# Optimization experiments

Hardware: AMD Instinct MI355X
Metric: run time of the kernel (lower is better)

Reference implementation:

```python
import jax, jax.numpy as jnp
import numpy as np

B, S, DIN, DIM = 4, 4096, 256, 256
GAMMA = 0.9865


def setup_inputs() -> dict:
    key = jax.random.key(0)
    ks = jax.random.split(key, 9)
    inp = {
        'xq': jax.random.normal(ks[0], (B, S, DIN), dtype=jnp.float32),
        'xk': jax.random.normal(ks[1], (B, S, DIN), dtype=jnp.float32),
        'xv': jax.random.normal(ks[2], (B, S, DIN), dtype=jnp.float32),
        'Wq': jax.random.normal(ks[3], (DIN, DIM), dtype=jnp.float32) * 0.05,
        'bq': jnp.zeros((DIM,), dtype=jnp.float32),
        'Wk': jax.random.normal(ks[4], (DIN, DIM), dtype=jnp.float32) * 0.05,
        'bk': jnp.zeros((DIM,), dtype=jnp.float32),
        'Wv': jax.random.normal(ks[5], (DIN, DIM), dtype=jnp.float32) * 0.05,
        'bv': jnp.zeros((DIM,), dtype=jnp.float32),
    }
    return inp


def _decay_matrix(s, gamma):
    # D[i, j] = gamma^(i-j) if i >= j else 0
    idx = jnp.arange(s)
    diff = idx[:, None] - idx[None, :]
    D = jnp.where(diff >= 0,
                  jnp.power(jnp.float32(gamma), diff.astype(jnp.float32)),
                  jnp.float32(0.0))
    return D


def reference(xq, xk, xv, Wq, bq, Wk, bk, Wv, bv):
    Q = xq @ Wq + bq  # [B,S,D]
    K = xk @ Wk + bk  # [B,S,D]
    V = xv @ Wv + bv  # [B,S,D]
    d = Q.shape[-1]
    # scores[b,i,j] = Q[b,i] . K[b,j] / sqrt(d)
    x = jnp.einsum('bid,bjd->bij', Q, K) / jnp.sqrt(jnp.float32(d))
    D = _decay_matrix(S, GAMMA)
    # Faithful to TF broadcasting: divides along the LAST axis (per-column by
    # sqrt of that index's row-sum): D[i,j] /= sqrt(sum_k D[j,k])
    D = D / jnp.sqrt(jnp.sum(D, axis=-1))
    x = x * D  # broadcast [B,S,S] * [S,S]
    # _norm_3 per batch element with TF broadcasting: x[b,i,j] /= max(|sum_k x[b,j,k]|, 1)
    denom = jnp.maximum(jnp.abs(jnp.sum(x, axis=-1)), 1.0)  # [B,S]
    x = x / denom[:, None, :]
    return x @ V  # [B,S,D]
```

## Files before the change

kernel.cpp:

```cpp
#include <hip/hip_runtime.h>
#include <math.h>

#define BB 4
#define SS 4096
#define DD 256
#define LL 256
#define NCH 16
#define GAMMA 0.9865f
#define LOG2G (-0.019609034f)
#define INV1MG 74.07407407f
#define SLAB 1032
#define SLABB 520

typedef __attribute__((ext_vector_type(8))) short short8;
typedef __attribute__((ext_vector_type(4))) float f32x4;
typedef unsigned short u16;
typedef unsigned int u32;

__device__ __forceinline__ u16 f2bf(float f) {
  union { float f; unsigned u; } v; v.f = f;
  unsigned r = v.u + 0x7FFFu + ((v.u >> 16) & 1u);
  return (u16)(r >> 16);
}
__device__ __forceinline__ float bf2f(u16 h) {
  union { unsigned u; float f; } v; v.u = ((unsigned)h) << 16; return v.f;
}

__device__ __forceinline__ void gll16(const u16* g, u16* l) {
  __builtin_amdgcn_global_load_lds(
      (const __attribute__((address_space(1))) u32*)g,
      (__attribute__((address_space(3))) u32*)l, 16, 0, 0);
}
__device__ __forceinline__ void stage8kp(const u16* g, u16* l, int lane) {
#pragma unroll
  for (int i = 0; i < 8; ++i)
    gll16(g + i * 512 + lane * 8, l + (i >> 1) * SLAB + (i & 1) * 512);
}

__device__ __forceinline__ void mfma_step_regB(
    const u16* Ah, const u16* Al, const short8 bh[4], const short8 bl[4],
    int wm0, int fm, int fq, f32x4 acc[4][4])
{
  const int ka = fq * SLAB;
  short8 ah[4], al[4];
#pragma unroll
  for (int i = 0; i < 4; ++i) {
    ah[i] = *(const short8*)&Ah[ka + (wm0 + i * 16 + fm) * 8];
    al[i] = *(const short8*)&Al[ka + (wm0 + i * 16 + fm) * 8];
  }
#pragma unroll
  for (int j = 0; j < 4; ++j)
#pragma unroll
    for (int i = 0; i < 4; ++i) {
      acc[i][j] = __builtin_amdgcn_mfma_f32_16x16x32_bf16(al[i], bh[j], acc[i][j], 0, 0, 0);
      acc[i][j] = __builtin_amdgcn_mfma_f32_16x16x32_bf16(ah[i], bl[j], acc[i][j], 0, 0, 0);
      acc[i][j] = __builtin_amdgcn_mfma_f32_16x16x32_bf16(ah[i], bh[j], acc[i][j], 0, 0, 0);
    }
}

__device__ __forceinline__ void mfma_step_regB_ab(
    const u16* Ah, const u16* Al, const short8 bh[2], const short8 bl[2],
    int wm0, int fm, int fq, f32x4 acc[4][2])
{
  const int ka = fq * SLAB;
  short8 ah[4], al[4];
#pragma unroll
  for (int i = 0; i < 4; ++i) {
    ah[i] = *(const short8*)&Ah[ka + (wm0 + i * 16 + fm) * 8];
    al[i] = *(const short8*)&Al[ka + (wm0 + i * 16 + fm) * 8];
  }
#pragma unroll
  for (int j = 0; j < 2; ++j)
#pragma unroll
    for (int i = 0; i < 4; ++i) {
      acc[i][j] = __builtin_amdgcn_mfma_f32_16x16x32_bf16(al[i], bh[j], acc[i][j], 0, 0, 0);
      acc[i][j] = __builtin_amdgcn_mfma_f32_16x16x32_bf16(ah[i], bl[j], acc[i][j], 0, 0, 0);
      acc[i][j] = __builtin_amdgcn_mfma_f32_16x16x32_bf16(ah[i], bh[j], acc[i][j], 0, 0, 0);
    }
}

__device__ __forceinline__ void loadBW(short8 bh[4], short8 bl[4],
    const u16* WhP, const u16* WlP, int ks, int wn0, int fm, int fq)
{
  const int base = ks * 4096 + fq * 1024;
#pragma unroll
  for (int j = 0; j < 4; ++j) {
    int o = base + (wn0 + j * 16 + fm) * 8;
    bh[j] = *(const short8*)&WhP[o];
    bl[j] = *(const short8*)&WlP[o];
  }
}
__device__ __forceinline__ void loadB2(short8 bh[2], short8 bl[2],
    const u16* BhP, const u16* BlP, int ks, int wn0, int fm, int fq)
{
  const int base = ks * 4096 + fq * 1024;
#pragma unroll
  for (int j = 0; j < 2; ++j) {
    int o = base + (wn0 + j * 16 + fm) * 8;
    bh[j] = *(const short8*)&BhP[o];
    bl[j] = *(const short8*)&BlP[o];
  }
}

__device__ __forceinline__ void mfma_step_ab(
    const u16* Ah, const u16* Al, const u16* Bh, const u16* Bl,
    int wm0, int wn0, int fm, int fq, f32x4 acc[4][2])
{
  const int ka = fq * SLAB, kb = fq * SLABB;
  short8 ah[4], al[4];
#pragma unroll
  for (int i = 0; i < 4; ++i) {
    ah[i] = *(const short8*)&Ah[ka + (wm0 + i * 16 + fm) * 8];
    al[i] = *(const short8*)&Al[ka + (wm0 + i * 16 + fm) * 8];
  }
#pragma unroll
  for (int j = 0; j < 2; ++j) {
    short8 bh = *(const short8*)&Bh[kb + (wn0 + j * 16 + fm) * 8];
    short8 bl = *(const short8*)&Bl[kb + (wn0 + j * 16 + fm) * 8];
#pragma unroll
    for (int i = 0; i < 4; ++i) {
      acc[i][j] = __builtin_amdgcn_mfma_f32_16x16x32_bf16(al[i], bh, acc[i][j], 0, 0, 0);
      acc[i][j] = __builtin_amdgcn_mfma_f32_16x16x32_bf16(ah[i], bl, acc[i][j], 0, 0, 0);
      acc[i][j] = __builtin_amdgcn_mfma_f32_16x16x32_bf16(ah[i], bh, acc[i][j], 0, 0, 0);
    }
  }
}

__device__ __forceinline__ void bounce_write(
    float* fb, const f32x4 acc[4][4], int wm0, int wn0, int fm, int fq, int p)
{
  if (wn0 == p * 64) {
#pragma unroll
    for (int i = 0; i < 4; ++i)
#pragma unroll
      for (int j = 0; j < 4; ++j)
#pragma unroll
        for (int r = 0; r < 4; ++r)
          fb[(wm0 + i * 16 + fq * 4 + r) * 65 + j * 16 + fm] = acc[i][j][r];
  }
}

__global__ __launch_bounds__(256) void init_pack_kernel(
    const float* __restrict__ Wq, const float* __restrict__ Wk, const float* __restrict__ Wv,
    u16* __restrict__ Wth, u16* __restrict__ Wtl,
    float* __restrict__ rsP, float* __restrict__ lVec)
{
  const int which = blockIdx.x;
  const int it = blockIdx.y;
  const int t = threadIdx.x;
  if (which == 0) {
    *(float4*)&rsP[(size_t)(it * 256 + t) * 4] = (float4){0.f, 0.f, 0.f, 0.f};
  } else if (which == 1) {
    *(float4*)&lVec[(size_t)(it * 256 + t) * 4] = (float4){0.f, 0.f, 0.f, 0.f};
  }
  const float* W = which == 0 ? Wq : (which == 1 ? Wk : Wv);
  for (int pn = 0; pn < 2; ++pn) {
    int pos = it * 256 + t;
    int k8 = pos >> 7, r = pos & 127;
    u16 hs[8], ls[8];
#pragma unroll
    for (int u = 0; u < 8; ++u) {
      float x = W[(size_t)(k8 * 8 + u) * DD + pn * 128 + r];
      u16 h = f2bf(x); hs[u] = h; ls[u] = f2bf(x - bf2f(h));
    }
    size_t o = ((size_t)((which * 2 + pn) * 32 + k8)) * 1024 + (size_t)r * 8;
    *(short8*)&Wth[o] = *(short8*)hs;
    *(short8*)&Wtl[o] = *(short8*)ls;
  }
}

__device__ __forceinline__ void loadX(float xs[2][8], const float* XP, int ks,
                                      int arow, int ak8) {
#pragma unroll
  for (int t = 0; t < 2; ++t) {
    const float* src = XP + (size_t)(t * 64 + arow) * DD + ks * 32 + ak8 * 8;
    *(float4*)&xs[t][0] = *(const float4*)src;
    *(float4*)&xs[t][4] = *(const float4*)(src + 4);
  }
}
__device__ __forceinline__ void writeAsplit(u16* Ab, const float xs[2][8],
                                            int arow, int ak8) {
#pragma unroll
  for (int t = 0; t < 2; ++t) {
    int row = t * 64 + arow;
    u16 hs[8], ls[8];
#pragma unroll
    for (int u = 0; u < 8; ++u) {
      u16 h = f2bf(xs[t][u]); hs[u] = h; ls[u] = f2bf(xs[t][u] - bf2f(h));
    }
    *(short8*)&Ab[ak8 * SLAB + row * 8] = *(short8*)hs;
    *(short8*)&Ab[4 * SLAB + ak8 * SLAB + row * 8] = *(short8*)ls;
  }
}

__global__ __launch_bounds__(256, 3) void proj_kernel(
    const float* __restrict__ xq, const float* __restrict__ xk, const float* __restrict__ xv,
    const u16* __restrict__ Wth, const u16* __restrict__ Wtl,
    const float* __restrict__ bq, const float* __restrict__ bk_, const float* __restrict__ bv,
    u16* __restrict__ Qh, u16* __restrict__ Ql,
    u16* __restrict__ Kh, u16* __restrict__ Kl,
    u16* __restrict__ KTh, u16* __restrict__ KTl, float* __restrict__ VT32,
    float* __restrict__ lVec)
{
  const int which = blockIdx.z;
  const float* bias = which == 0 ? bq : (which == 1 ? bk_ : bv);
  const int m0 = blockIdx.x * 128;
  const int pn = blockIdx.y;
  __shared__ u16 SM[16 * SLAB + 128];
  __shared__ float rsc[128];
  __shared__ float wlut[128];
  __shared__ float kacc[64];
  float* fb = (float*)SM;
  const int tid = threadIdx.x, lane = tid & 63, wave = tid >> 6;
  const int wm0 = (wave >> 1) * 64, wn0 = (wave & 1) * 64;
  const int fm = lane & 15, fq = lane >> 4;
  if (which == 1) {
    if (tid < 128) {
      int sb = (m0 & (SS - 1)) + tid;
      rsc[tid] = rsqrtf((1.0f - exp2f((float)(sb + 1) * LOG2G)) * INV1MG);
      wlut[tid] = exp2f((float)(255 - ((m0 & (LL - 1)) + tid)) * LOG2G);
    }
    if (tid < 64) kacc[tid] = 0.f;
  }
  const float* XP = (which == 0 ? xq : (which == 1 ? xk : xv)) + (size_t)m0 * DD;
  const u16* WhP = Wth + (size_t)((which * 2 + pn) * 32) * 1024;
  const u16* WlP = Wtl + (size_t)((which * 2 + pn) * 32) * 1024;
  const int arow = tid >> 2, ak8 = tid & 3;
  f32x4 acc[4][4];
#pragma unroll
  for (int i = 0; i < 4; ++i)
#pragma unroll
    for (int j = 0; j < 4; ++j) acc[i][j] = (f32x4){0.f, 0.f, 0.f, 0.f};
  float xs[2][8];
  short8 bh[4], bl[4];
  loadBW(bh, bl, WhP, WlP, 0, wn0, fm, fq);
  loadX(xs, XP, 0, arow, ak8);
  writeAsplit(SM, xs, arow, ak8);
  int cur = 0;
  for (int ks = 0; ks < 8; ++ks) {
    __syncthreads();
    u16* Ac = SM + cur * 8 * SLAB;
    u16* An = SM + (cur ^ 1) * 8 * SLAB;
    if (ks < 7) loadX(xs, XP, ks + 1, arow, ak8);
    mfma_step_regB(Ac, Ac + 4 * SLAB, bh, bl, wm0, fm, fq, acc);
    if (ks < 7) {
      loadBW(bh, bl, WhP, WlP, ks + 1, wn0, fm, fq);
      writeAsplit(An, xs, arow, ak8);
    }
    cur ^= 1;
  }
  const int b = m0 >> 12, sbb = m0 & (SS - 1);
  for (int p = 0; p < 2; ++p) {
    __syncthreads();
    bounce_write(fb, acc, wm0, wn0, fm, fq, p);
    __syncthreads();
    if (which == 0) {
#pragma unroll
      for (int it = 0; it < 4; ++it) {
        int unit = it * 256 + tid;
        int k8l = unit >> 7, row = unit & 127;
        int gcol0 = pn * 128 + p * 64 + k8l * 8;
        u16 hs[8], ls[8];
#pragma unroll
        for (int u = 0; u < 8; ++u) {
          float v = (fb[row * 65 + k8l * 8 + u] + bias[gcol0 + u]) * (1.f / 16.f);
          u16 h = f2bf(v); hs[u] = h; ls[u] = f2bf(v - bf2f(h));
        }
        size_t o = (size_t)(m0 >> 7) * 32768 + (size_t)(pn * 16 + p * 8 + k8l) * 1024 + row * 8;
        *(short8*)&Qh[o] = *(short8*)hs;
        *(short8*)&Ql[o] = *(short8*)ls;
      }
    } else if (which == 1) {
#pragma unroll
      for (int it = 0; it < 4; ++it) {
        int unit = it * 256 + tid;
        int k8l = unit >> 7, row = unit & 127;
        int gcol0 = pn * 128 + p * 64 + k8l * 8;
        u16 hs[8], ls[8];
#pragma unroll
        for (int u = 0; u < 8; ++u) {
          float v = (fb[row * 65 + k8l * 8 + u] + bias[gcol0 + u]) * rsc[row];
          u16 h = f2bf(v); hs[u] = h; ls[u] = f2bf(v - bf2f(h));
        }
        size_t o = (size_t)(m0 >> 7) * 32768 + (size_t)(pn * 16 + p * 8 + k8l) * 1024 + row * 8;
        *(short8*)&Kh[o] = *(short8*)hs;
        *(short8*)&Kl[o] = *(short8*)ls;
      }
      float kpart = 0.f;
#pragma unroll
      for (int it = 0; it < 4; ++it) {
        int unit = it * 256 + tid;
        int dl = unit & 63, s8l = unit >> 6;
        int gcolg = pn * 128 + p * 64 + dl;
        float bs = bias[gcolg];
        u16 hs[8], ls[8];
#pragma unroll
        for (int u = 0; u < 8; ++u) {
          int row = s8l * 8 + u;
          float v = (fb[row * 65 + dl] + bs) * rsc[row];
          kpart = fmaf(v, wlut[row], kpart);
          u16 h = f2bf(v); hs[u] = h; ls[u] = f2bf(v - bf2f(h));
        }
        int sb0 = sbb + s8l * 8;
        size_t o = ((size_t)(b * 2 + (gcolg >> 7)) * 512 + (sb0 >> 3)) * 1024 + (size_t)(gcolg & 127) * 8;
        *(short8*)&KTh[o] = *(short8*)hs;
        *(short8*)&KTl[o] = *(short8*)ls;
      }
      atomicAdd(&kacc[tid & 63], kpart);
      __syncthreads();
      if (tid < 64) {
        int c = sbb >> 8;
        atomicAdd(&lVec[(size_t)(b * NCH + c) * DD + pn * 128 + p * 64 + tid], kacc[tid]);
        kacc[tid] = 0.f;
      }
    } else {
#pragma unroll
      for (int it = 0; it < 4; ++it) {
        int unit = it * 256 + tid;
        int dl = unit & 63, s8l = unit >> 6;
        int gcolg = pn * 128 + p * 64 + dl;
        float bs = bias[gcolg];
        float vv[8];
#pragma unroll
        for (int u = 0; u < 8; ++u) vv[u] = fb[(s8l * 8 + u) * 65 + dl] + bs;
        float* dst = &VT32[(size_t)b * DD * SS + (size_t)gcolg * SS + sbb + s8l * 8];
        *(float4*)dst = (float4){vv[0], vv[1], vv[2], vv[3]};
        *(float4*)(dst + 4) = (float4){vv[4], vv[5], vv[6], vv[7]};
      }
    }
  }
}

__global__ __launch_bounds__(256, 4) void scores_kernel(
    const u16* __restrict__ Qh, const u16* __restrict__ Ql,
    const u16* __restrict__ Kh, const u16* __restrict__ Kl,
    const float* __restrict__ lVec, u16* __restrict__ Sgh, u16* __restrict__ Sgl,
    float* __restrict__ rsP)
{
  const int chunk = blockIdx.x, b = chunk >> 4, c = chunk & 15;
  const int y = blockIdx.y;
  const int m0 = (y < 2) ? 0 : 128;
  const int jn0 = (y < 2) ? y * 64 : (y - 2) * 64;
  __shared__ u16 SA[2 * 8 * SLAB];
  __shared__ float cv[256], lut[256], rowAcc[128], qd2[2][128];
  float* fb = (float*)SA;
  const int tid = threadIdx.x, lane = tid & 63, wave = tid >> 6;
  const int wm0 = (wave >> 1) * 64, wn0 = (wave & 1) * 32;
  const int fm = lane & 15, fq = lane >> 4;
  if (jn0 == 0) {
    const float gL = exp2f((float)LL * LOG2G);
    float s = 0.f;
    for (int cp = 0; cp < c; ++cp)
      s = fmaf(gL, s, lVec[(size_t)(b * NCH + cp) * DD + tid]);
    cv[tid] = s;
  }
  lut[tid] = exp2f((float)tid * LOG2G);
  if (tid < 128) rowAcc[tid] = 0.f;
  const int growA = b * SS + c * LL + m0;
  const int growB = b * SS + c * LL + jn0;
  const u16* QhP = Qh + (size_t)(growA >> 7) * 32768;
  const u16* QlP = Ql + (size_t)(growA >> 7) * 32768;
  const u16* KhP = Kh + (size_t)(growB >> 7) * 32768 + (size_t)(growB & 127) * 8;
  const u16* KlP = Kl + (size_t)(growB >> 7) * 32768 + (size_t)(growB & 127) * 8;
  f32x4 acc[4][2];
#pragma unroll
  for (int i = 0; i < 4; ++i)
#pragma unroll
    for (int j = 0; j < 2; ++j) acc[i][j] = (f32x4){0.f, 0.f, 0.f, 0.f};
  float qdreg = 0.f;
  const int qrow = tid & 127, qk8b = tid >> 7;
  short8 bh[2], bl[2];
  if (wave == 0) stage8kp(QhP, SA, lane);
  if (wave == 1) stage8kp(QlP, SA + 4 * SLAB, lane);
  loadB2(bh, bl, KhP, KlP, 0, wn0, fm, fq);
  int cur = 0;
  for (int ks = 0; ks < 8; ++ks) {
    __syncthreads();
    u16* Ac = cur ? SA + 8 * SLAB : SA;
    u16* An = cur ? SA : SA + 8 * SLAB;
    if (ks < 7) {
      if (wave == 0) stage8kp(QhP + (ks + 1) * 4096, An, lane);
      if (wave == 1) stage8kp(QlP + (ks + 1) * 4096, An + 4 * SLAB, lane);
    }
    mfma_step_regB_ab(Ac, Ac + 4 * SLAB, bh, bl, wm0, fm, fq, acc);
    if (ks < 7) loadB2(bh, bl, KhP, KlP, ks + 1, wn0, fm, fq);
    if (jn0 == 0) {
#pragma unroll
      for (int h2 = 0; h2 < 2; ++h2) {
        int k8l = qk8b + 2 * h2;
        const u16* ahp = &Ac[k8l * SLAB + qrow * 8];
        const u16* alp = &Ac[4 * SLAB + k8l * SLAB + qrow * 8];
#pragma unroll
        for (int u = 0; u < 8; ++u)
          qdreg = fmaf(bf2f(ahp[u]) + bf2f(alp[u]), cv[ks * 32 + k8l * 8 + u], qdreg);
      }
    }
    cur ^= 1;
  }
  qd2[qk8b][qrow] = qdreg;
  const int ps = chunk * 2 + (m0 >> 7);
  for (int rh = 0; rh < 2; ++rh) {
    __syncthreads();
    if (wm0 == rh * 64) {
#pragma unroll
      for (int i = 0; i < 4; ++i)
#pragma unroll
        for (int j = 0; j < 2; ++j)
#pragma unroll
          for (int r = 0; r < 4; ++r)
            fb[(i * 16 + fq * 4 + r) * 65 + wn0 + j * 16 + fm] = acc[i][j][r];
    }
    __syncthreads();
#pragma unroll
    for (int it = 0; it < 2; ++it) {
      int unit = it * 256 + tid;
      int k8l = unit >> 6, rowl = unit & 63;
      int il = m0 + rh * 64 + rowl;
      int jlb = jn0 + k8l * 8;
      float part = 0.f;
      u16 hs[8], ls[8];
#pragma unroll
      for (int u = 0; u < 8; ++u) {
        int jl = jlb + u;
        float v = (jl <= il) ? fb[rowl * 65 + k8l * 8 + u] * lut[il - jl] : 0.f;
        part += v;
        u16 h = f2bf(v); hs[u] = h; ls[u] = f2bf(v - bf2f(h));
      }
      atomicAdd(&rowAcc[rh * 64 + rowl], part);
      size_t o = (size_t)(ps * 32 + (jn0 >> 3) + k8l) * 1024 + (size_t)(rh * 64 + rowl) * 8;
      *(short8*)&Sgh[o] = *(short8*)hs;
      *(short8*)&Sgl[o] = *(short8*)ls;
    }
  }
  __syncthreads();
  if (tid < 128) {
    float rs = rowAcc[tid];
    if (jn0 == 0)
      rs += exp2f((float)(m0 + tid + 1) * LOG2G) * (qd2[0][tid] + qd2[1][tid]);
    atomicAdd(&rsP[(size_t)b * SS + c * LL + m0 + tid], rs);
  }
}

__global__ __launch_bounds__(256, 4) void lmat_kernel(
    const float* __restrict__ VT32, const float* __restrict__ rsP,
    const u16* __restrict__ KTh, const u16* __restrict__ KTl,
    float* __restrict__ lMatT)
{
  const int chunk = blockIdx.x, b = chunk >> 4, c = chunk & 15;
  const int ty = blockIdx.y;
  const int m0 = (ty >> 2) * 128, n0 = (ty & 3) * 64;
  __shared__ u16 SA[2 * 8 * SLAB];
  __shared__ float swl[256];
  const int tid = threadIdx.x, lane = tid & 63, wave = tid >> 6;
  const int wm0 = (wave >> 1) * 64, wn0 = (wave & 1) * 32;
  const int fm = lane & 15, fq = lane >> 4;
  swl[tid] = exp2f((float)(255 - tid) * LOG2G) /
             fmaxf(fabsf(rsP[(size_t)b * SS + c * LL + tid]), 1.0f);
  const float* AP = VT32 + (size_t)b * DD * SS + (size_t)m0 * SS + c * LL;
  const u16* BhP = KTh + ((size_t)(b * 2 + (n0 >> 7)) * 512 + c * 32) * 1024 + (size_t)(n0 & 127) * 8;
  const u16* BlP = KTl + ((size_t)(b * 2 + (n0 >> 7)) * 512 + c * 32) * 1024 + (size_t)(n0 & 127) * 8;
  const int arow = tid >> 1;
  f32x4 acc[4][2];
#pragma unroll
  for (int i = 0; i < 4; ++i)
#pragma unroll
    for (int j = 0; j < 2; ++j) acc[i][j] = (f32x4){0.f, 0.f, 0.f, 0.f};
  float as[2][8];
  short8 bh[2], bl[2];
  loadB2(bh, bl, BhP, BlP, 0, wn0, fm, fq);
#pragma unroll
  for (int t = 0; t < 2; ++t) {
    int ak8 = (tid & 1) * 2 + t;
    const float* src = AP + (size_t)arow * SS + ak8 * 8;
    *(float4*)&as[t][0] = *(const float4*)src;
    *(float4*)&as[t][4] = *(const float4*)(src + 4);
  }
  __syncthreads();
#pragma unroll
  for (int t = 0; t < 2; ++t) {
    int ak8 = (tid & 1) * 2 + t;
    u16 hs[8], ls[8];
#pragma unroll
    for (int u = 0; u < 8; ++u) {
      float v = as[t][u] * swl[ak8 * 8 + u];
      u16 h = f2bf(v); hs[u] = h; ls[u] = f2bf(v - bf2f(h));
    }
    *(short8*)&SA[ak8 * SLAB + arow * 8] = *(short8*)hs;
    *(short8*)&SA[4 * SLAB + ak8 * SLAB + arow * 8] = *(short8*)ls;
  }
  int cur = 0;
  for (int ks = 0; ks < 8; ++ks) {
    __syncthreads();
    u16* Ac = cur ? SA + 8 * SLAB : SA;
    u16* An = cur ? SA : SA + 8 * SLAB;
    if (ks < 7) {
#pragma unroll
      for (int t = 0; t < 2; ++t) {
        int ak8 = (tid & 1) * 2 + t;
        const float* src = AP + (size_t)arow * SS + (ks + 1) * 32 + ak8 * 8;
        *(float4*)&as[t][0] = *(const float4*)src;
        *(float4*)&as[t][4] = *(const float4*)(src + 4);
      }
    }
    mfma_step_regB_ab(Ac, Ac + 4 * SLAB, bh, bl, wm0, fm, fq, acc);
    if (ks < 7) {
      loadB2(bh, bl, BhP, BlP, ks + 1, wn0, fm, fq);
#pragma unroll
      for (int t = 0; t < 2; ++t) {
        int ak8 = (tid & 1) * 2 + t;
        u16 hs[8], ls[8];
#pragma unroll
        for (int u = 0; u < 8; ++u) {
          float v = as[t][u] * swl[(ks + 1) * 32 + ak8 * 8 + u];
          u16 h = f2bf(v); hs[u] = h; ls[u] = f2bf(v - bf2f(h));
        }
        *(short8*)&An[ak8 * SLAB + arow * 8] = *(short8*)hs;
        *(short8*)&An[4 * SLAB + ak8 * SLAB + arow * 8] = *(short8*)ls;
      }
    }
    cur ^= 1;
  }
#pragma unroll
  for (int i = 0; i < 4; ++i)
#pragma unroll
    for (int j = 0; j < 2; ++j)
#pragma unroll
      for (int r = 0; r < 4; ++r) {
        int e = m0 + wm0 + i * 16 + fq * 4 + r;
        int d = n0 + wn0 + j * 16 + fm;
        lMatT[(size_t)chunk * 65536 + (size_t)e * 256 + d] = acc[i][j][r];
      }
}

__global__ __launch_bounds__(256) void combine_mat_kernel(
    const float* __restrict__ lMatT, u16* __restrict__ cMh, u16* __restrict__ cMl)
{
  const int t = blockIdx.x * 256 + threadIdx.x;
  const int b = t >> 13, rem = t & 8191;
  const int k8 = rem >> 8, e = rem & 255;
  const float gL = powf(GAMMA, (float)LL);
  float s[8] = {0.f, 0.f, 0.f, 0.f, 0.f, 0.f, 0.f, 0.f};
  for (int ch = 0; ch < 16; ++ch) {
    size_t ro = (size_t)(b * 16 + ch) * 65536 + (size_t)e * 256 + k8 * 8;
    float4 a0 = *(const float4*)&lMatT[ro];
    float4 a1 = *(const float4*)&lMatT[ro + 4];
    float vals[8] = {a0.x, a0.y, a0.z, a0.w, a1.x, a1.y, a1.z, a1.w};
    u16 hh[8], ll[8];
#pragma unroll
    for (int u = 0; u < 8; ++u) {
      u16 h = f2bf(s[u]); hh[u] = h; ll[u] = f2bf(s[u] - bf2f(h));
    }
    size_t wo = ((size_t)(((b * 16 + ch) * 2 + (e >> 7)) * 32 + k8)) * 1024 + (size_t)(e & 127) * 8;
    *(short8*)&cMh[wo] = *(short8*)hh;
    *(short8*)&cMl[wo] = *(short8*)ll;
#pragma unroll
    for (int u = 0; u < 8; ++u) s[u] = gL * s[u] + vals[u];
  }
}

__global__ __launch_bounds__(256, 3) void out_kernel(
    const u16* __restrict__ Qh, const u16* __restrict__ Ql,
    const u16* __restrict__ cMh, const u16* __restrict__ cMl,
    const u16* __restrict__ Sgh, const u16* __restrict__ Sgl,
    const float* __restrict__ VT32, const float* __restrict__ rsP,
    float* __restrict__ out)
{
  const int chunk = blockIdx.x, b = chunk >> 4, c = chunk & 15;
  const int ty = blockIdx.y;
  const int m0 = (ty >> 2) * 128, n0 = (ty & 3) * 64;
  __shared__ u16 SA[2 * 8 * SLAB];
  __shared__ u16 SB[2 * 8 * SLABB];
  __shared__ float olut[128];
  __shared__ float sdn[256];
  const int tid = threadIdx.x, lane = tid & 63, wave = tid >> 6;
  const int wm0 = (wave >> 1) * 64, wn0 = (wave & 1) * 32;
  const int fm = lane & 15, fq = lane >> 4;
  if (tid < 128) olut[tid] = exp2f((float)(m0 + tid + 1) * LOG2G);
  sdn[tid] = 1.0f / fmaxf(fabsf(rsP[(size_t)b * SS + c * LL + tid]), 1.0f);
  f32x4 acc[4][2];
#pragma unroll
  for (int i = 0; i < 4; ++i)
#pragma unroll
    for (int j = 0; j < 2; ++j) acc[i][j] = (f32x4){0.f, 0.f, 0.f, 0.f};
  int cur = 0;
  {
    const u16* AhP = Qh + (size_t)(b * 32 + c * 2 + (m0 >> 7)) * 32768;
    const u16* AlP = Ql + (size_t)(b * 32 + c * 2 + (m0 >> 7)) * 32768;
    const u16* BhP = cMh + (size_t)(chunk * 2 + (n0 >> 7)) * 32768 + (size_t)(n0 & 127) * 8;
    const u16* BlP = cMl + (size_t)(chunk * 2 + (n0 >> 7)) * 32768 + (size_t)(n0 & 127) * 8;
    short8 bh[2], bl[2];
    if (wave == 0) stage8kp(AhP, SA, lane);
    if (wave == 1) stage8kp(AlP, SA + 4 * SLAB, lane);
    loadB2(bh, bl, BhP, BlP, 0, wn0, fm, fq);
    for (int ks = 0; ks < 8; ++ks) {
      __syncthreads();
      u16* Ac = cur ? SA + 8 * SLAB : SA;
      u16* An = cur ? SA : SA + 8 * SLAB;
      if (ks < 7) {
        if (wave == 0) stage8kp(AhP + (ks + 1) * 4096, An, lane);
        if (wave == 1) stage8kp(AlP + (ks + 1) * 4096, An + 4 * SLAB, lane);
      }
      mfma_step_regB_ab(Ac, Ac + 4 * SLAB, bh, bl, wm0, fm, fq, acc);
      if (ks < 7) loadB2(bh, bl, BhP, BlP, ks + 1, wn0, fm, fq);
      cur ^= 1;
    }
  }
  {
    const u16* AhP = Sgh + (size_t)(chunk * 2 + (m0 >> 7)) * 32768;
    const u16* AlP = Sgl + (size_t)(chunk * 2 + (m0 >> 7)) * 32768;
    const float* BP = VT32 + (size_t)b * DD * SS + (size_t)n0 * SS + c * LL;
    const int ber = tid >> 2, bk8 = tid & 3;
    const int nks = (m0 >> 5) + 4;
    float bs[8];
    {
      u16* Ac = cur ? SA + 8 * SLAB : SA;
      u16* Bc = cur ? SB + 8 * SLABB : SB;
      if (wave == 0) stage8kp(AhP, Ac, lane);
      if (wave == 1) stage8kp(AlP, Ac + 4 * SLAB, lane);
      const float* src = BP + (size_t)ber * SS + bk8 * 8;
      *(float4*)&bs[0] = *(const float4*)src;
      *(float4*)&bs[4] = *(const float4*)(src + 4);
#pragma unroll
      for (int i = 0; i < 4; ++i)
#pragma unroll
        for (int r = 0; r < 4; ++r) {
          int rl = wm0 + i * 16 + fq * 4 + r;
          float sc = olut[rl];
#pragma unroll
          for (int j = 0; j < 2; ++j) acc[i][j][r] *= sc;
        }
      u16 hs[8], ls[8];
#pragma unroll
      for (int u = 0; u < 8; ++u) {
        float v = bs[u] * sdn[bk8 * 8 + u];
        u16 h = f2bf(v); hs[u] = h; ls[u] = f2bf(v - bf2f(h));
      }
      *(short8*)&Bc[bk8 * SLABB + ber * 8] = *(short8*)hs;
      *(short8*)&Bc[4 * SLABB + bk8 * SLABB + ber * 8] = *(short8*)ls;
    }
    for (int ks = 0; ks < nks; ++ks) {
      __syncthreads();
      u16* Ac = cur ? SA + 8 * SLAB : SA;
      u16* Bc = cur ? SB + 8 * SLABB : SB;
      u16* An = cur ? SA : SA + 8 * SLAB;
      u16* Bn = cur ? SB : SB + 8 * SLABB;
      if (ks + 1 < nks) {
        if (wave == 0) stage8kp(AhP + (ks + 1) * 4096, An, lane);
        if (wave == 1) stage8kp(AlP + (ks + 1) * 4096, An + 4 * SLAB, lane);
        const float* src = BP + (size_t)ber * SS + (ks + 1) * 32 + bk8 * 8;
        *(float4*)&bs[0] = *(const float4*)src;
        *(float4*)&bs[4] = *(const float4*)(src + 4);
      }
      mfma_step_ab(Ac, Ac + 4 * SLAB, Bc, Bc + 4 * SLABB, wm0, wn0, fm, fq, acc);
      if (ks + 1 < nks) {
        u16 hs[8], ls[8];
#pragma unroll
        for (int u = 0; u < 8; ++u) {
          float v = bs[u] * sdn[(ks + 1) * 32 + bk8 * 8 + u];
          u16 h = f2bf(v); hs[u] = h; ls[u] = f2bf(v - bf2f(h));
        }
        *(short8*)&Bn[bk8 * SLABB + ber * 8] = *(short8*)hs;
        *(short8*)&Bn[4 * SLABB + bk8 * SLABB + ber * 8] = *(short8*)ls;
      }
      cur ^= 1;
    }
  }
#pragma unroll
  for (int i = 0; i < 4; ++i)
#pragma unroll
    for (int j = 0; j < 2; ++j)
#pragma unroll
      for (int r = 0; r < 4; ++r) {
        int il = m0 + wm0 + i * 16 + fq * 4 + r;
        int e = n0 + wn0 + j * 16 + fm;
        out[(size_t)(b * SS + c * LL + il) * DD + e] = acc[i][j][r];
      }
}

extern "C" void kernel_launch(void* const* d_in, const int* in_sizes, int n_in,
                              void* d_out, int out_size, void* d_ws, size_t ws_size,
                              hipStream_t stream) {
  const float* xq = (const float*)d_in[0];
  const float* xk = (const float*)d_in[1];
  const float* xv = (const float*)d_in[2];
  const float* Wq = (const float*)d_in[3];
  const float* bq = (const float*)d_in[4];
  const float* Wk = (const float*)d_in[5];
  const float* bk = (const float*)d_in[6];
  const float* Wv = (const float*)d_in[7];
  const float* bv = (const float*)d_in[8];
  float* out = (float*)d_out;

  char* p = (char*)d_ws;
  const size_t H16 = (size_t)BB * SS * DD * 2;
  u16* Qh   = (u16*)(p + 0 * H16);  u16* Ql   = (u16*)(p + 1 * H16);
  u16* Kh   = (u16*)(p + 2 * H16);  u16* Kl   = (u16*)(p + 3 * H16);
  u16* KTh  = (u16*)(p + 4 * H16);  u16* KTl  = (u16*)(p + 5 * H16);
  u16* Sgh  = (u16*)(p + 10 * H16); u16* Sgl  = (u16*)(p + 11 * H16);
  u16* cMh  = (u16*)(p + 12 * H16); u16* cMl  = (u16*)(p + 13 * H16);
  float* lMatT = (float*)(p + 14 * H16);
  float* VT32  = (float*)(p + 16 * H16);
  u16* Wth = (u16*)(p + 18 * H16);
  u16* Wtl = (u16*)(p + 18 * H16 + 3 * DD * DD * 2);
  float* rsP  = (float*)(p + 18 * H16 + 6 * DD * DD * 2);
  float* lVec = rsP + (size_t)BB * SS;

  init_pack_kernel<<<dim3(3, 16), 256, 0, stream>>>(Wq, Wk, Wv, Wth, Wtl, rsP, lVec);
  proj_kernel<<<dim3(BB * SS / 128, 2, 3), 256, 0, stream>>>(
      xq, xk, xv, Wth, Wtl, bq, bk, bv, Qh, Ql, Kh, Kl, KTh, KTl, VT32, lVec);
  scores_kernel<<<dim3(BB * NCH, 6), 256, 0, stream>>>(
      Qh, Ql, Kh, Kl, lVec, Sgh, Sgl, rsP);
  lmat_kernel<<<dim3(BB * NCH, 8), 256, 0, stream>>>(VT32, rsP, KTh, KTl, lMatT);
  combine_mat_kernel<<<128, 256, 0, stream>>>(lMatT, cMh, cMl);
  out_kernel<<<dim3(BB * NCH, 8), 256, 0, stream>>>(
      Qh, Ql, cMh, cMl, Sgh, Sgl, VT32, rsP, out);
}
```

Baseline: 198.2 us.

## Deepen global-load prefetch to two stages and use lighter LDS barriers in GEMM loops

```diff
diff --git a/kernel.cpp b/kernel.cpp
--- a/kernel.cpp
+++ b/kernel.cpp
@@ -17,6 +17,8 @@
 typedef unsigned short u16;
 typedef unsigned int u32;
 
+#define BARK() asm volatile("s_waitcnt lgkmcnt(0)\n\ts_barrier" ::: "memory")
+
 __device__ __forceinline__ u16 f2bf(float f) {
   union { float f; unsigned u; } v; v.f = f;
   unsigned r = v.u + 0x7FFFu + ((v.u >> 16) & 1u);
@@ -190,6 +192,31 @@
     }
     *(short8*)&Ab[ak8 * SLAB + row * 8] = *(short8*)hs;
     *(short8*)&Ab[4 * SLAB + ak8 * SLAB + row * 8] = *(short8*)ls;
+  }
+}
+__device__ __forceinline__ void loadA2(float as[2][8], const float* AP, int ks,
+                                       int arow, int tid) {
+#pragma unroll
+  for (int t = 0; t < 2; ++t) {
+    int ak8 = (tid & 1) * 2 + t;
+    const float* src = AP + (size_t)arow * SS + ks * 32 + ak8 * 8;
+    *(float4*)&as[t][0] = *(const float4*)src;
+    *(float4*)&as[t][4] = *(const float4*)(src + 4);
+  }
+}
+__device__ __forceinline__ void writeA2(u16* Ab, const float as[2][8],
+                                        const float* swl, int ks, int arow, int tid) {
+#pragma unroll
+  for (int t = 0; t < 2; ++t) {
+    int ak8 = (tid & 1) * 2 + t;
+    u16 hs[8], ls[8];
+#pragma unroll
+    for (int u = 0; u < 8; ++u) {
+      float v = as[t][u] * swl[ks * 32 + ak8 * 8 + u];
+      u16 h = f2bf(v); hs[u] = h; ls[u] = f2bf(v - bf2f(h));
+    }
+    *(short8*)&Ab[ak8 * SLAB + arow * 8] = *(short8*)hs;
+    *(short8*)&Ab[4 * SLAB + ak8 * SLAB + arow * 8] = *(short8*)ls;
   }
 }
 
@@ -231,23 +258,26 @@
   for (int i = 0; i < 4; ++i)
 #pragma unroll
     for (int j = 0; j < 4; ++j) acc[i][j] = (f32x4){0.f, 0.f, 0.f, 0.f};
-  float xs[2][8];
+  float xsA[2][8], xsB[2][8];
   short8 bh[4], bl[4];
   loadBW(bh, bl, WhP, WlP, 0, wn0, fm, fq);
-  loadX(xs, XP, 0, arow, ak8);
-  writeAsplit(SM, xs, arow, ak8);
-  int cur = 0;
-  for (int ks = 0; ks < 8; ++ks) {
-    __syncthreads();
-    u16* Ac = SM + cur * 8 * SLAB;
-    u16* An = SM + (cur ^ 1) * 8 * SLAB;
-    if (ks < 7) loadX(xs, XP, ks + 1, arow, ak8);
-    mfma_step_regB(Ac, Ac + 4 * SLAB, bh, bl, wm0, fm, fq, acc);
-    if (ks < 7) {
-      loadBW(bh, bl, WhP, WlP, ks + 1, wn0, fm, fq);
-      writeAsplit(An, xs, arow, ak8);
-    }
-    cur ^= 1;
+  loadX(xsA, XP, 0, arow, ak8);
+  loadX(xsB, XP, 1, arow, ak8);
+  writeAsplit(SM, xsA, arow, ak8);
+  loadX(xsA, XP, 2, arow, ak8);
+  for (int k2 = 0; k2 < 4; ++k2) {
+    BARK();
+    mfma_step_regB(SM, SM + 4 * SLAB, bh, bl, wm0, fm, fq, acc);
+    loadBW(bh, bl, WhP, WlP, 2 * k2 + 1, wn0, fm, fq);
+    writeAsplit(SM + 8 * SLAB, xsB, arow, ak8);
+    if (k2 < 3) loadX(xsB, XP, 2 * k2 + 3, arow, ak8);
+    BARK();
+    mfma_step_regB(SM + 8 * SLAB, SM + 12 * SLAB, bh, bl, wm0, fm, fq, acc);
+    if (k2 < 3) {
+      loadBW(bh, bl, WhP, WlP, 2 * k2 + 2, wn0, fm, fq);
+      writeAsplit(SM, xsA, arow, ak8);
+      if (k2 < 2) loadX(xsA, XP, 2 * k2 + 4, arow, ak8);
+    }
   }
   const int b = m0 >> 12, sbb = m0 & (SS - 1);
   for (int p = 0; p < 2; ++p) {
@@ -465,60 +495,27 @@
   for (int i = 0; i < 4; ++i)
 #pragma unroll
     for (int j = 0; j < 2; ++j) acc[i][j] = (f32x4){0.f, 0.f, 0.f, 0.f};
-  float as[2][8];
+  float asA[2][8], asB[2][8];
   short8 bh[2], bl[2];
   loadB2(bh, bl, BhP, BlP, 0, wn0, fm, fq);
-#pragma unroll
-  for (int t = 0; t < 2; ++t) {
-    int ak8 = (tid & 1) * 2 + t;
-    const float* src = AP + (size_t)arow * SS + ak8 * 8;
-    *(float4*)&as[t][0] = *(const float4*)src;
-    *(float4*)&as[t][4] = *(const float4*)(src + 4);
-  }
+  loadA2(asA, AP, 0, arow, tid);
+  loadA2(asB, AP, 1, arow, tid);
   __syncthreads();
-#pragma unroll
-  for (int t = 0; t < 2; ++t) {
-    int ak8 = (tid & 1) * 2 + t;
-    u16 hs[8], ls[8];
-#pragma unroll
-    for (int u = 0; u < 8; ++u) {
-      float v = as[t][u] * swl[ak8 * 8 + u];
-      u16 h = f2bf(v); hs[u] = h; ls[u] = f2bf(v - bf2f(h));
-    }
-    *(short8*)&SA[ak8 * SLAB + arow * 8] = *(short8*)hs;
-    *(short8*)&SA[4 * SLAB + ak8 * SLAB + arow * 8] = *(short8*)ls;
-  }
-  int cur = 0;
-  for (int ks = 0; ks < 8; ++ks) {
-    __syncthreads();
-    u16* Ac = cur ? SA + 8 * SLAB : SA;
-    u16* An = cur ? SA : SA + 8 * SLAB;
-    if (ks < 7) {
-#pragma unroll
-      for (int t = 0; t < 2; ++t) {
-        int ak8 = (tid & 1) * 2 + t;
-        const float* src = AP + (size_t)arow * SS + (ks + 1) * 32 + ak8 * 8;
-        *(float4*)&as[t][0] = *(const float4*)src;
-        *(float4*)&as[t][4] = *(const float4*)(src + 4);
-      }
-    }
-    mfma_step_regB_ab(Ac, Ac + 4 * SLAB, bh, bl, wm0, fm, fq, acc);
-    if (ks < 7) {
-      loadB2(bh, bl, BhP, BlP, ks + 1, wn0, fm, fq);
-#pragma unroll
-      for (int t = 0; t < 2; ++t) {
-        int ak8 = (tid & 1) * 2 + t;
-        u16 hs[8], ls[8];
-#pragma unroll
-        for (int u = 0; u < 8; ++u) {
-          float v = as[t][u] * swl[(ks + 1) * 32 + ak8 * 8 + u];
-          u16 h = f2bf(v); hs[u] = h; ls[u] = f2bf(v - bf2f(h));
-        }
-        *(short8*)&An[ak8 * SLAB + arow * 8] = *(short8*)hs;
-        *(short8*)&An[4 * SLAB + ak8 * SLAB + arow * 8] = *(short8*)ls;
-      }
-    }
-    cur ^= 1;
+  writeA2(SA, asA, swl, 0, arow, tid);
+  loadA2(asA, AP, 2, arow, tid);
+  for (int k2 = 0; k2 < 4; ++k2) {
+    BARK();
+    mfma_step_regB_ab(SA, SA + 4 * SLAB, bh, bl, wm0, fm, fq, acc);
+    loadB2(bh, bl, BhP, BlP, 2 * k2 + 1, wn0, fm, fq);
+    writeA2(SA + 8 * SLAB, asB, swl, 2 * k2 + 1, arow, tid);
+    if (k2 < 3) loadA2(asB, AP, 2 * k2 + 3, arow, tid);
+    BARK();
+    mfma_step_regB_ab(SA + 8 * SLAB, SA + 12 * SLAB, bh, bl, wm0, fm, fq, acc);
+    if (k2 < 3) {
+      loadB2(bh, bl, BhP, BlP, 2 * k2 + 2, wn0, fm, fq);
+      writeA2(SA, asA, swl, 2 * k2 + 2, arow, tid);
+      if (k2 < 2) loadA2(asA, AP, 2 * k2 + 4, arow, tid);
+    }
   }
 #pragma unroll
   for (int i = 0; i < 4; ++i)
```

Result: slower. 266.4 us (+34.4%).

## Load MFMA operands directly from global into registers, dropping LDS staging

Applied to the files above, without the earlier changes.

```diff
diff --git a/kernel.cpp b/kernel.cpp
--- a/kernel.cpp
+++ b/kernel.cpp
@@ -10,7 +10,6 @@
 #define LOG2G (-0.019609034f)
 #define INV1MG 74.07407407f
 #define SLAB 1032
-#define SLABB 520
 
 typedef __attribute__((ext_vector_type(8))) short short8;
 typedef __attribute__((ext_vector_type(4))) float f32x4;
@@ -25,16 +24,13 @@
 __device__ __forceinline__ float bf2f(u16 h) {
   union { unsigned u; float f; } v; v.u = ((unsigned)h) << 16; return v.f;
 }
-
-__device__ __forceinline__ void gll16(const u16* g, u16* l) {
-  __builtin_amdgcn_global_load_lds(
-      (const __attribute__((address_space(1))) u32*)g,
-      (__attribute__((address_space(3))) u32*)l, 16, 0, 0);
-}
-__device__ __forceinline__ void stage8kp(const u16* g, u16* l, int lane) {
-#pragma unroll
-  for (int i = 0; i < 8; ++i)
-    gll16(g + i * 512 + lane * 8, l + (i >> 1) * SLAB + (i & 1) * 512);
+__device__ __forceinline__ void split8(const float v[8], short8* h8, short8* l8) {
+  u16 hs[8], ls[8];
+#pragma unroll
+  for (int u = 0; u < 8; ++u) {
+    u16 h = f2bf(v[u]); hs[u] = h; ls[u] = f2bf(v[u] - bf2f(h));
+  }
+  *h8 = *(short8*)hs; *l8 = *(short8*)ls;
 }
 
 __device__ __forceinline__ void mfma_step_regB(
@@ -58,17 +54,10 @@
     }
 }
 
-__device__ __forceinline__ void mfma_step_regB_ab(
-    const u16* Ah, const u16* Al, const short8 bh[2], const short8 bl[2],
-    int wm0, int fm, int fq, f32x4 acc[4][2])
-{
-  const int ka = fq * SLAB;
-  short8 ah[4], al[4];
-#pragma unroll
-  for (int i = 0; i < 4; ++i) {
-    ah[i] = *(const short8*)&Ah[ka + (wm0 + i * 16 + fm) * 8];
-    al[i] = *(const short8*)&Al[ka + (wm0 + i * 16 + fm) * 8];
-  }
+__device__ __forceinline__ void mfma_regs_ab(
+    const short8 ah[4], const short8 al[4],
+    const short8 bh[2], const short8 bl[2], f32x4 acc[4][2])
+{
 #pragma unroll
   for (int j = 0; j < 2; ++j)
 #pragma unroll
@@ -79,6 +68,17 @@
     }
 }
 
+__device__ __forceinline__ void loadA4(short8 ah[4], short8 al[4],
+    const u16* AhP, const u16* AlP, int ks, int wm0, int fm, int fq)
+{
+  const int base = ks * 4096 + fq * 1024;
+#pragma unroll
+  for (int i = 0; i < 4; ++i) {
+    int o = base + (wm0 + i * 16 + fm) * 8;
+    ah[i] = *(const short8*)&AhP[o];
+    al[i] = *(const short8*)&AlP[o];
+  }
+}
 __device__ __forceinline__ void loadBW(short8 bh[4], short8 bl[4],
     const u16* WhP, const u16* WlP, int ks, int wn0, int fm, int fq)
 {
@@ -99,30 +99,6 @@
     int o = base + (wn0 + j * 16 + fm) * 8;
     bh[j] = *(const short8*)&BhP[o];
     bl[j] = *(const short8*)&BlP[o];
-  }
-}
-
-__device__ __forceinline__ void mfma_step_ab(
-    const u16* Ah, const u16* Al, const u16* Bh, const u16* Bl,
-    int wm0, int wn0, int fm, int fq, f32x4 acc[4][2])
-{
-  const int ka = fq * SLAB, kb = fq * SLABB;
-  short8 ah[4], al[4];
-#pragma unroll
-  for (int i = 0; i < 4; ++i) {
-    ah[i] = *(const short8*)&Ah[ka + (wm0 + i * 16 + fm) * 8];
-    al[i] = *(const short8*)&Al[ka + (wm0 + i * 16 + fm) * 8];
-  }
-#pragma unroll
-  for (int j = 0; j < 2; ++j) {
-    short8 bh = *(const short8*)&Bh[kb + (wn0 + j * 16 + fm) * 8];
-    short8 bl = *(const short8*)&Bl[kb + (wn0 + j * 16 + fm) * 8];
-#pragma unroll
-    for (int i = 0; i < 4; ++i) {
-      acc[i][j] = __builtin_amdgcn_mfma_f32_16x16x32_bf16(al[i], bh, acc[i][j], 0, 0, 0);
-      acc[i][j] = __builtin_amdgcn_mfma_f32_16x16x32_bf16(ah[i], bl, acc[i][j], 0, 0, 0);
-      acc[i][j] = __builtin_amdgcn_mfma_f32_16x16x32_bf16(ah[i], bh, acc[i][j], 0, 0, 0);
-    }
   }
 }
 
@@ -341,9 +317,8 @@
   const int y = blockIdx.y;
   const int m0 = (y < 2) ? 0 : 128;
   const int jn0 = (y < 2) ? y * 64 : (y - 2) * 64;
-  __shared__ u16 SA[2 * 8 * SLAB];
+  __shared__ float fb[64 * 65];
   __shared__ float cv[256], lut[256], rowAcc[128], qd2[2][128];
-  float* fb = (float*)SA;
   const int tid = threadIdx.x, lane = tid & 63, wave = tid >> 6;
   const int wm0 = (wave >> 1) * 64, wn0 = (wave & 1) * 32;
   const int fm = lane & 15, fq = lane >> 4;
@@ -369,33 +344,24 @@
     for (int j = 0; j < 2; ++j) acc[i][j] = (f32x4){0.f, 0.f, 0.f, 0.f};
   float qdreg = 0.f;
   const int qrow = tid & 127, qk8b = tid >> 7;
-  short8 bh[2], bl[2];
-  if (wave == 0) stage8kp(QhP, SA, lane);
-  if (wave == 1) stage8kp(QlP, SA + 4 * SLAB, lane);
-  loadB2(bh, bl, KhP, KlP, 0, wn0, fm, fq);
-  int cur = 0;
+  __syncthreads();
   for (int ks = 0; ks < 8; ++ks) {
-    __syncthreads();
-    u16* Ac = cur ? SA + 8 * SLAB : SA;
-    u16* An = cur ? SA : SA + 8 * SLAB;
-    if (ks < 7) {
-      if (wave == 0) stage8kp(QhP + (ks + 1) * 4096, An, lane);
-      if (wave == 1) stage8kp(QlP + (ks + 1) * 4096, An + 4 * SLAB, lane);
-    }
-    mfma_step_regB_ab(Ac, Ac + 4 * SLAB, bh, bl, wm0, fm, fq, acc);
-    if (ks < 7) loadB2(bh, bl, KhP, KlP, ks + 1, wn0, fm, fq);
+    short8 ah[4], al[4], bh[2], bl[2];
+    loadA4(ah, al, QhP, QlP, ks, wm0, fm, fq);
+    loadB2(bh, bl, KhP, KlP, ks, wn0, fm, fq);
+    mfma_regs_ab(ah, al, bh, bl, acc);
     if (jn0 == 0) {
 #pragma unroll
       for (int h2 = 0; h2 < 2; ++h2) {
         int k8l = qk8b + 2 * h2;
-        const u16* ahp = &Ac[k8l * SLAB + qrow * 8];
-        const u16* alp = &Ac[4 * SLAB + k8l * SLAB + qrow * 8];
+        short8 hv = *(const short8*)&QhP[ks * 4096 + k8l * 1024 + qrow * 8];
+        short8 lv = *(const short8*)&QlP[ks * 4096 + k8l * 1024 + qrow * 8];
 #pragma unroll
         for (int u = 0; u < 8; ++u)
-          qdreg = fmaf(bf2f(ahp[u]) + bf2f(alp[u]), cv[ks * 32 + k8l * 8 + u], qdreg);
-      }
-    }
-    cur ^= 1;
+          qdreg = fmaf(bf2f((u16)hv[u]) + bf2f((u16)lv[u]),
+                       cv[ks * 32 + k8l * 8 + u], qdreg);
+      }
+    }
   }
   qd2[qk8b][qrow] = qdreg;
   const int ps = chunk * 2 + (m0 >> 7);
@@ -449,7 +415,6 @@
   const int chunk = blockIdx.x, b = chunk >> 4, c = chunk & 15;
   const int ty = blockIdx.y;
   const int m0 = (ty >> 2) * 128, n0 = (ty & 3) * 64;
-  __shared__ u16 SA[2 * 8 * SLAB];
   __shared__ float swl[256];
   const int tid = threadIdx.x, lane = tid & 63, wave = tid >> 6;
   const int wm0 = (wave >> 1) * 64, wn0 = (wave & 1) * 32;
@@ -459,66 +424,27 @@
   const float* AP = VT32 + (size_t)b * DD * SS + (size_t)m0 * SS + c * LL;
   const u16* BhP = KTh + ((size_t)(b * 2 + (n0 >> 7)) * 512 + c * 32) * 1024 + (size_t)(n0 & 127) * 8;
   const u16* BlP = KTl + ((size_t)(b * 2 + (n0 >> 7)) * 512 + c * 32) * 1024 + (size_t)(n0 & 127) * 8;
-  const int arow = tid >> 1;
   f32x4 acc[4][2];
 #pragma unroll
   for (int i = 0; i < 4; ++i)
 #pragma unroll
     for (int j = 0; j < 2; ++j) acc[i][j] = (f32x4){0.f, 0.f, 0.f, 0.f};
-  float as[2][8];
-  short8 bh[2], bl[2];
-  loadB2(bh, bl, BhP, BlP, 0, wn0, fm, fq);
-#pragma unroll
-  for (int t = 0; t < 2; ++t) {
-    int ak8 = (tid & 1) * 2 + t;
-    const float* src = AP + (size_t)arow * SS + ak8 * 8;
-    *(float4*)&as[t][0] = *(const float4*)src;
-    *(float4*)&as[t][4] = *(const float4*)(src + 4);
-  }
   __syncthreads();
-#pragma unroll
-  for (int t = 0; t < 2; ++t) {
-    int ak8 = (tid & 1) * 2 + t;
-    u16 hs[8], ls[8];
-#pragma unroll
-    for (int u = 0; u < 8; ++u) {
-      float v = as[t][u] * swl[ak8 * 8 + u];
-      u16 h = f2bf(v); hs[u] = h; ls[u] = f2bf(v - bf2f(h));
-    }
-    *(short8*)&SA[ak8 * SLAB + arow * 8] = *(short8*)hs;
-    *(short8*)&SA[4 * SLAB + ak8 * SLAB + arow * 8] = *(short8*)ls;
-  }
-  int cur = 0;
   for (int ks = 0; ks < 8; ++ks) {
-    __syncthreads();
-    u16* Ac = cur ? SA + 8 * SLAB : SA;
-    u16* An = cur ? SA : SA + 8 * SLAB;
-    if (ks < 7) {
-#pragma unroll
-      for (int t = 0; t < 2; ++t) {
-        int ak8 = (tid & 1) * 2 + t;
-        const float* src = AP + (size_t)arow * SS + (ks + 1) * 32 + ak8 * 8;
-        *(float4*)&as[t][0] = *(const float4*)src;
-        *(float4*)&as[t][4] = *(const float4*)(src + 4);
-      }
-    }
-    mfma_step_regB_ab(Ac, Ac + 4 * SLAB, bh, bl, wm0, fm, fq, acc);
-    if (ks < 7) {
-      loadB2(bh, bl, BhP, BlP, ks + 1, wn0, fm, fq);
-#pragma unroll
-      for (int t = 0; t < 2; ++t) {
-        int ak8 = (tid & 1) * 2 + t;
-        u16 hs[8], ls[8];
-#pragma unroll
-        for (int u = 0; u < 8; ++u) {
-          float v = as[t][u] * swl[(ks + 1) * 32 + ak8 * 8 + u];
-          u16 h = f2bf(v); hs[u] = h; ls[u] = f2bf(v - bf2f(h));
-        }
-        *(short8*)&An[ak8 * SLAB + arow * 8] = *(short8*)hs;
-        *(short8*)&An[4 * SLAB + ak8 * SLAB + arow * 8] = *(short8*)ls;
-      }
-    }
-    cur ^= 1;
+    float4 sw0 = *(const float4*)&swl[ks * 32 + fq * 8];
+    float4 sw1 = *(const float4*)&swl[ks * 32 + fq * 8 + 4];
+    short8 ah[4], al[4], bh[2], bl[2];
+#pragma unroll
+    for (int i = 0; i < 4; ++i) {
+      const float* src = AP + (size_t)(wm0 + i * 16 + fm) * SS + ks * 32 + fq * 8;
+      float4 a0 = *(const float4*)src;
+      float4 a1 = *(const float4*)(src + 4);
+      float v[8] = {a0.x * sw0.x, a0.y * sw0.y, a0.z * sw0.z, a0.w * sw0.w,
+                    a1.x * sw1.x, a1.y * sw1.y, a1.z * sw1.z, a1.w * sw1.w};
+      split8(v, &ah[i], &al[i]);
+    }
+    loadB2(bh, bl, BhP, BlP, ks, wn0, fm, fq);
+    mfma_regs_ab(ah, al, bh, bl, acc);
   }
 #pragma unroll
   for (int i = 0; i < 4; ++i)
@@ -558,7 +484,7 @@
   }
 }
 
-__global__ __launch_bounds__(256, 3) void out_kernel(
+__global__ __launch_bounds__(256, 4) void out_kernel(
     const u16* __restrict__ Qh, const u16* __restrict__ Ql,
     const u16* __restrict__ cMh, const u16* __restrict__ cMl,
     const u16* __restrict__ Sgh, const u16* __restrict__ Sgl,
@@ -568,8 +494,6 @@
   const int chunk = blockIdx.x, b = chunk >> 4, c = chunk & 15;
   const int ty = blockIdx.y;
   const int m0 = (ty >> 2) * 128, n0 = (ty & 3) * 64;
-  __shared__ u16 SA[2 * 8 * SLAB];
-  __shared__ u16 SB[2 * 8 * SLABB];
   __shared__ float olut[128];
   __shared__ float sdn[256];
   const int tid = threadIdx.x, lane = tid & 63, wave = tid >> 6;
@@ -582,87 +506,48 @@
   for (int i = 0; i < 4; ++i)
 #pragma unroll
     for (int j = 0; j < 2; ++j) acc[i][j] = (f32x4){0.f, 0.f, 0.f, 0.f};
-  int cur = 0;
+  __syncthreads();
   {
     const u16* AhP = Qh + (size_t)(b * 32 + c * 2 + (m0 >> 7)) * 32768;
     const u16* AlP = Ql + (size_t)(b * 32 + c * 2 + (m0 >> 7)) * 32768;
     const u16* BhP = cMh + (size_t)(chunk * 2 + (n0 >> 7)) * 32768 + (size_t)(n0 & 127) * 8;
     const u16* BlP = cMl + (size_t)(chunk * 2 + (n0 >> 7)) * 32768 + (size_t)(n0 & 127) * 8;
-    short8 bh[2], bl[2];
-    if (wave == 0) stage8kp(AhP, SA, lane);
-    if (wave == 1) stage8kp(AlP, SA + 4 * SLAB, lane);
-    loadB2(bh, bl, BhP, BlP, 0, wn0, fm, fq);
     for (int ks = 0; ks < 8; ++ks) {
-      __syncthreads();
-      u16* Ac = cur ? SA + 8 * SLAB : SA;
-      u16* An = cur ? SA : SA + 8 * SLAB;
-      if (ks < 7) {
-        if (wave == 0) stage8kp(AhP + (ks + 1) * 4096, An, lane);
-        if (wave == 1) stage8kp(AlP + (ks + 1) * 4096, An + 4 * SLAB, lane);
-      }
-      mfma_step_regB_ab(Ac, Ac + 4 * SLAB, bh, bl, wm0, fm, fq, acc);
-      if (ks < 7) loadB2(bh, bl, BhP, BlP, ks + 1, wn0, fm, fq);
-      cur ^= 1;
-    }
-  }
+      short8 ah[4], al[4], bh[2], bl[2];
+      loadA4(ah, al, AhP, AlP, ks, wm0, fm, fq);
+      loadB2(bh, bl, BhP, BlP, ks, wn0, fm, fq);
+      mfma_regs_ab(ah, al, bh, bl, acc);
+    }
+  }
+#pragma unroll
+  for (int i = 0; i < 4; ++i)
+#pragma unroll
+    for (int r = 0; r < 4; ++r) {
+      int rl = wm0 + i * 16 + fq * 4 + r;
+      float sc = olut[rl];
+#pragma unroll
+      for (int j = 0; j < 2; ++j) acc[i][j][r] *= sc;
+    }
   {
     const u16* AhP = Sgh + (size_t)(chunk * 2 + (m0 >> 7)) * 32768;
     const u16* AlP = Sgl + (size_t)(chunk * 2 + (m0 >> 7)) * 32768;
     const float* BP = VT32 + (size_t)b * DD * SS + (size_t)n0 * SS + c * LL;
-    const int ber = tid >> 2, bk8 = tid & 3;
     const int nks = (m0 >> 5) + 4;
-    float bs[8];
-    {
-      u16* Ac = cur ? SA + 8 * SLAB : SA;
-      u16* Bc = cur ? SB + 8 * SLABB : SB;
-      if (wave == 0) stage8kp(AhP, Ac, lane);
-      if (wave == 1) stage8kp(AlP, Ac + 4 * SLAB, lane);
-      const float* src = BP + (size_t)ber * SS + bk8 * 8;
-      *(float4*)&bs[0] = *(const float4*)src;
-      *(float4*)&bs[4] = *(const float4*)(src + 4);
-#pragma unroll
-      for (int i = 0; i < 4; ++i)
-#pragma unroll
-        for (int r = 0; r < 4; ++r) {
-          int rl = wm0 + i * 16 + fq * 4 + r;
-          float sc = olut[rl];
-#pragma unroll
-          for (int j = 0; j < 2; ++j) acc[i][j][r] *= sc;
-        }
-      u16 hs[8], ls[8];
-#pragma unroll
-      for (int u = 0; u < 8; ++u) {
-        float v = bs[u] * sdn[bk8 * 8 + u];
-        u16 h = f2bf(v); hs[u] = h; ls[u] = f2bf(v - bf2f(h));
-      }
-      *(short8*)&Bc[bk8 * SLABB + ber * 8] = *(short8*)hs;
-      *(short8*)&Bc[4 * SLABB + bk8 * SLABB + ber * 8] = *(short8*)ls;
-    }
     for (int ks = 0; ks < nks; ++ks) {
-      __syncthreads();
-      u16* Ac = cur ? SA + 8 * SLAB : SA;
-      u16* Bc = cur ? SB + 8 * SLABB : SB;
-      u16* An = cur ? SA : SA + 8 * SLAB;
-      u16* Bn = cur ? SB : SB + 8 * SLABB;
-      if (ks + 1 < nks) {
-        if (wave == 0) stage8kp(AhP + (ks + 1) * 4096, An, lane);
-        if (wave == 1) stage8kp(AlP + (ks + 1) * 4096, An + 4 * SLAB, lane);
-        const float* src = BP + (size_t)ber * SS + (ks + 1) * 32 + bk8 * 8;
-        *(float4*)&bs[0] = *(const float4*)src;
-        *(float4*)&bs[4] = *(const float4*)(src + 4);
-      }
-      mfma_step_ab(Ac, Ac + 4 * SLAB, Bc, Bc + 4 * SLABB, wm0, wn0, fm, fq, acc);
-      if (ks + 1 < nks) {
-        u16 hs[8], ls[8];
-#pragma unroll
-        for (int u = 0; u < 8; ++u) {
-          float v = bs[u] * sdn[(ks + 1) * 32 + bk8 * 8 + u];
-          u16 h = f2bf(v); hs[u] = h; ls[u] = f2bf(v - bf2f(h));
-        }
-        *(short8*)&Bn[bk8 * SLABB + ber * 8] = *(short8*)hs;
-        *(short8*)&Bn[4 * SLABB + bk8 * SLABB + ber * 8] = *(short8*)ls;
-      }
-      cur ^= 1;
+      float4 sd0 = *(const float4*)&sdn[ks * 32 + fq * 8];
+      float4 sd1 = *(const float4*)&sdn[ks * 32 + fq * 8 + 4];
+      short8 ah[4], al[4], bh[2], bl[2];
+      loadA4(ah, al, AhP, AlP, ks, wm0, fm, fq);
+#pragma unroll
+      for (int j = 0; j < 2; ++j) {
+        const float* src = BP + (size_t)(wn0 + j * 16 + fm) * SS + ks * 32 + fq * 8;
+        float4 b0 = *(const float4*)src;
+        float4 b1 = *(const float4*)(src + 4);
+        float v[8] = {b0.x * sd0.x, b0.y * sd0.y, b0.z * sd0.z, b0.w * sd0.w,
+                      b1.x * sd1.x, b1.y * sd1.y, b1.z * sd1.z, b1.w * sd1.w};
+        split8(v, &bh[j], &bl[j]);
+      }
+      mfma_regs_ab(ah, al, bh, bl, acc);
     }
   }
 #pragma unroll
```

Measured after the change: 216.4 us. 9.2% more time.
